# Kernel optimization log

Measured on AMD Instinct MI355X. Metric: run time of the kernel, lower is better.

Reference implementation:

```python
import jax, jax.numpy as jnp
import numpy as np

B, T, D_MODEL = 4, 8192, 1024
D_K, D_V = 128, 128
DILATIONS = [1, 2, 4, 8]
SEG = 128                      # segment_count for every head
NORM = 1.0 / np.sqrt(D_K)      # norm_fact = 1/sqrt(d_k)
H = len(DILATIONS)


def setup_inputs() -> dict:
    key = jax.random.key(0)
    ks = jax.random.split(key, 6)
    x = jax.random.normal(ks[0], (B, T, D_MODEL), dtype=jnp.float32)
    # head weights, init like torch: randn(k, m)/sqrt(k), stacked over heads
    Wk = jax.random.normal(ks[1], (H, D_K, D_MODEL), dtype=jnp.float32) / np.sqrt(D_K)
    Wq = jax.random.normal(ks[2], (H, D_K, D_MODEL), dtype=jnp.float32) / np.sqrt(D_K)
    Wv = jax.random.normal(ks[3], (H, D_V, D_MODEL), dtype=jnp.float32) / np.sqrt(D_V)
    # output projection (concat of H heads -> d_model), torch Linear layout (out, in)
    W_out = jax.random.normal(ks[4], (D_MODEL, H * D_V), dtype=jnp.float32) / np.sqrt(H * D_V)
    b_out = jnp.zeros((D_MODEL,), dtype=jnp.float32)
    return {"x": x, "Wk": Wk, "Wq": Wq, "Wv": Wv, "W_out": W_out, "b_out": b_out}


def _head(x, wk, wq, wv, dil):
    """SingleHeadDilatedSelfAttention with padding='same', is_causal=True."""
    Bb, Tt, E = x.shape
    nb = Tt // SEG                       # attention length before dilation
    # view(B, T//seg, seg, E).permute(0,2,3,1) -> (B, seg, E, nb); dilate last dim
    xv = x.reshape(Bb, nb, SEG, E).transpose(0, 2, 3, 1)[:, :, :, ::dil]  # (B, seg, E, L)
    Q = jnp.einsum('bsel,ke->bslk', xv, wq)   # (B, seg, L, d_k)
    K = jnp.einsum('bsel,ke->bslk', xv, wk)
    V = jnp.einsum('bsel,ve->bslv', xv, wv)   # (B, seg, L, d_v)
    # KQ[b,s,n,m]: n = key position, m = query position
    KQ = jnp.einsum('bsnd,bsmd->bsnm', K, Q)
    mask = jnp.tril(jnp.ones((nb, nb), dtype=bool))[::dil, ::dil]  # (L, L)
    KQ = jnp.where(mask, KQ, -jnp.inf)
    # original applies softmax along dim 3 (the query axis) of KQ * norm_fact
    smKQ = jax.nn.softmax(KQ * NORM, axis=3)
    att = jnp.einsum('bsnm,bsnv->bsmv', smKQ, V)   # (B, seg, L, d_v)
    L = att.shape[2]
    # 'same' padding: strided scatter back to full sequence length
    out = jnp.zeros((Bb, Tt, D_V), dtype=x.dtype)
    out = out.at[:, ::dil, :].set(att.reshape(Bb, SEG * L, D_V))
    return out


def reference(x, Wk, Wq, Wv, W_out, b_out):
    heads = [_head(x, Wk[h], Wq[h], Wv[h], DILATIONS[h]) for h in range(H)]
    cat = jnp.concatenate(heads, axis=-1)            # (B, T, H*d_v)
    return cat @ W_out.T + b_out                     # (B, T, d_model)
```

## Files before the change

### kernel.cpp

```cpp
#include <hip/hip_runtime.h>
#include <cstdint>
#include <cstddef>

typedef __attribute__((ext_vector_type(8))) short bf16x8;
typedef __attribute__((ext_vector_type(4))) float f32x4;

__device__ __forceinline__ unsigned short f2bf(float f) {
  union { float f; uint32_t u; } v; v.f = f;
  uint32_t r = v.u + 0x7fffu + ((v.u >> 16) & 1u);
  return (unsigned short)(r >> 16);
}
__device__ __forceinline__ float bf2f(unsigned short u) {
  union { uint32_t u; float f; } v; v.u = ((uint32_t)u) << 16;
  return v.f;
}

__device__ __forceinline__ void glds16(const void* g, void* l) {
  __builtin_amdgcn_global_load_lds(
      (const __attribute__((address_space(1))) unsigned int*)g,
      (__attribute__((address_space(3))) unsigned int*)l, 16, 0, 0);
}

__device__ __forceinline__ size_t head_off(int h) {
  return (size_t)65536 * ((h == 0) ? 0 : (h == 1) ? 64 : (h == 2) ? 96 : 112);
}

__global__ void k_cvt(const float* __restrict__ src, unsigned short* __restrict__ dst, int n4) {
  int i = blockIdx.x * 256 + threadIdx.x;
  if (i < n4) {
    float4 f = ((const float4*)src)[i];
    ushort4 u;
    u.x = f2bf(f.x); u.y = f2bf(f.y); u.z = f2bf(f.z); u.w = f2bf(f.w);
    ((ushort4*)dst)[i] = u;
  }
}

__global__ void k_cvt_w(const float* __restrict__ Wq, const float* __restrict__ Wk,
                        const float* __restrict__ Wv, unsigned short* __restrict__ dst) {
  int row = blockIdx.x;
  int h = row / 384, j = row % 384;
  const float* src = (j < 128) ? (Wq + (size_t)(h * 128 + j) * 1024)
                   : (j < 256) ? (Wk + (size_t)(h * 128 + j - 128) * 1024)
                               : (Wv + (size_t)(h * 128 + j - 256) * 1024);
  int e = threadIdx.x * 4;
  float4 f = *(const float4*)(src + e);
  ushort4 u;
  u.x = f2bf(f.x); u.y = f2bf(f.y); u.z = f2bf(f.z); u.w = f2bf(f.w);
  *(ushort4*)(dst + (size_t)row * 1024 + e) = u;
}

__global__ __launch_bounds__(256) void k_qkv(
    const unsigned short* __restrict__ xbf,
    const unsigned short* __restrict__ wbf,
    unsigned short* __restrict__ qws,
    unsigned short* __restrict__ kws,
    unsigned short* __restrict__ vws) {
  int i = blockIdx.x;
  int group = i / 24, jj = i - group * 24;
  int gy = jj >> 3, slot = jj & 7;
  int gx = group * 8 + slot;
  int h, base;
  if (gx < 256)      { h = 0; base = 0; }
  else if (gx < 384) { h = 1; base = 256; }
  else if (gx < 448) { h = 2; base = 384; }
  else               { h = 3; base = 448; }
  int L = 64 >> h, dil = 1 << h;
  int inner = gx - base;
  int b = inner >> (6 - h);
  int l = inner & (L - 1);
  const unsigned short* Abase = xbf + ((size_t)(b * 8192 + l * dil * 128)) * 1024;
  const unsigned short* Bbase = wbf + ((size_t)(h * 384 + gy * 128)) * 1024;

  __shared__ unsigned short As[128 * 64];
  __shared__ unsigned short Bs[128 * 64];

  int tid = threadIdx.x;
  int lane = tid & 63, wave = tid >> 6;
  int wm = wave >> 1, wn = wave & 1;
  int li = lane & 15, lk8 = (lane >> 4) << 3;

  int urow = tid >> 3;
  int uc8 = (tid & 7) << 3;

  f32x4 acc[4][4] = {};

  for (int kc = 0; kc < 1024; kc += 64) {
    __syncthreads();
#pragma unroll
    for (int it = 0; it < 4; ++it) {
      int row = it * 32 + urow;
      glds16(Abase + (size_t)row * 1024 + kc + uc8, &As[it * 2048 + wave * 512]);
      glds16(Bbase + (size_t)row * 1024 + kc + uc8, &Bs[it * 2048 + wave * 512]);
    }
    __syncthreads();
#pragma unroll
    for (int kk = 0; kk < 2; ++kk) {
      int k0 = kk * 32 + lk8;
      bf16x8 af[4], bfv[4];
#pragma unroll
      for (int mf = 0; mf < 4; ++mf)
        af[mf] = *(const bf16x8*)&As[(wm * 64 + mf * 16 + li) * 64 + k0];
#pragma unroll
      for (int nf = 0; nf < 4; ++nf)
        bfv[nf] = *(const bf16x8*)&Bs[(wn * 64 + nf * 16 + li) * 64 + k0];
#pragma unroll
      for (int mf = 0; mf < 4; ++mf)
#pragma unroll
        for (int nf = 0; nf < 4; ++nf)
          acc[mf][nf] = __builtin_amdgcn_mfma_f32_16x16x32_bf16(af[mf], bfv[nf], acc[mf][nf], 0, 0, 0);
    }
  }
  unsigned short* dst = ((gy == 0) ? qws : (gy == 1) ? kws : vws) + head_off(h);
  int ib = (lane >> 4) * 4;
#pragma unroll
  for (int mf = 0; mf < 4; ++mf) {
#pragma unroll
    for (int nf = 0; nf < 4; ++nf) {
#pragma unroll
      for (int rg = 0; rg < 4; ++rg) {
        int s = wm * 64 + mf * 16 + ib + rg;
        int j = wn * 64 + nf * 16 + li;
        dst[((size_t)((b * 128 + s) * L + l)) * 128 + j] = f2bf(acc[mf][nf][rg]);
      }
    }
  }
}

__global__ __launch_bounds__(256) void k_attn(
    const unsigned short* __restrict__ qws,
    const unsigned short* __restrict__ kws,
    const unsigned short* __restrict__ vws,
    unsigned short* __restrict__ att) {
  int bx = blockIdx.x;
  int h, inst;
  if (bx < 512)      { h = 0; inst = bx; }
  else if (bx < 768) { h = 1; inst = bx - 512; }
  else if (bx < 896) { h = 2; inst = bx - 768; }
  else               { h = 3; inst = bx - 896; }
  int lgL = 6 - h;
  int L = 64 >> h;
  int Lm1 = L - 1;
  int bpb = 128 >> h;
  int b = inst / bpb;
  int s0 = (inst % bpb) << h;
  size_t off0 = head_off(h) + ((size_t)(b * 128 + s0) * L) * 128;
  const unsigned short* Qg = qws + off0;
  const unsigned short* Kg = kws + off0;
  const unsigned short* Vg = vws + off0;
  unsigned short* Og = att + off0;

  __shared__ unsigned short PT[64][72];
  __shared__ unsigned short VtL[128][72];

  int tid = threadIdx.x;
  int lane = tid & 63, w = tid >> 6;
  int li = lane & 15, q = lane >> 4;
  int lk8 = q << 3;

#pragma unroll
  for (int c = 0; c < 4; ++c) {
    int u = tid + c * 256;
    int n = u & 63, vblk = u >> 6;
    bf16x8 ve = *(const bf16x8*)(Vg + n * 128 + vblk * 8);
#pragma unroll
    for (int j = 0; j < 8; ++j)
      VtL[vblk * 8 + j][n] = (unsigned short)ve[j];
  }

  f32x4 sacc[4] = {};
  int nrow = 16 * w + li;
  for (int kc = 0; kc < 4; ++kc) {
    int d0 = kc * 32 + lk8;
    bf16x8 af = *(const bf16x8*)(Kg + nrow * 128 + d0);
#pragma unroll
    for (int mt = 0; mt < 4; ++mt) {
      bf16x8 bfq = *(const bf16x8*)(Qg + (mt * 16 + li) * 128 + d0);
      sacc[mt] = __builtin_amdgcn_mfma_f32_16x16x32_bf16(af, bfq, sacc[mt], 0, 0, 0);
    }
  }

  float sv[4][4];
#pragma unroll
  for (int mt = 0; mt < 4; ++mt)
#pragma unroll
    for (int r = 0; r < 4; ++r) {
      int n = 16 * w + 4 * q + r;
      int m = mt * 16 + li;
      bool valid = ((m >> lgL) == (n >> lgL)) && ((m & Lm1) <= (n & Lm1));
      sv[mt][r] = valid ? sacc[mt][r] * 0.08838834764831845f : -1e30f;
    }
  float inv[4];
#pragma unroll
  for (int r = 0; r < 4; ++r) {
    float m0 = fmaxf(fmaxf(sv[0][r], sv[1][r]), fmaxf(sv[2][r], sv[3][r]));
#pragma unroll
    for (int d = 1; d < 16; d <<= 1)
      m0 = fmaxf(m0, __shfl_xor(m0, d, 64));
    float s0 = 0.f;
#pragma unroll
    for (int mt = 0; mt < 4; ++mt) {
      sv[mt][r] = __expf(sv[mt][r] - m0);
      s0 += sv[mt][r];
    }
#pragma unroll
    for (int d = 1; d < 16; d <<= 1)
      s0 += __shfl_xor(s0, d, 64);
    inv[r] = 1.f / s0;
  }

#pragma unroll
  for (int mt = 0; mt < 4; ++mt) {
    ushort4 pk;
    pk.x = f2bf(sv[mt][0] * inv[0]);
    pk.y = f2bf(sv[mt][1] * inv[1]);
    pk.z = f2bf(sv[mt][2] * inv[2]);
    pk.w = f2bf(sv[mt][3] * inv[3]);
    *(ushort4*)&PT[mt * 16 + li][16 * w + 4 * q] = pk;
  }
  __syncthreads();

  f32x4 oacc[8] = {};
#pragma unroll
  for (int ks = 0; ks < 2; ++ks) {
    int n0 = ks * 32 + lk8;
    bf16x8 af = *(const bf16x8*)&PT[16 * w + li][n0];
#pragma unroll
    for (int vt = 0; vt < 8; ++vt) {
      bf16x8 bfv = *(const bf16x8*)&VtL[vt * 16 + li][n0];
      oacc[vt] = __builtin_amdgcn_mfma_f32_16x16x32_bf16(af, bfv, oacc[vt], 0, 0, 0);
    }
  }
#pragma unroll
  for (int vt = 0; vt < 8; ++vt) {
#pragma unroll
    for (int r = 0; r < 4; ++r) {
      int m = 16 * w + 4 * q + r;
      int v = vt * 16 + li;
      Og[m * 128 + v] = f2bf(oacc[vt][r]);
    }
  }
}

__global__ __launch_bounds__(256) void k_out(
    const unsigned short* __restrict__ att,
    const unsigned short* __restrict__ wout,
    const float* __restrict__ bout,
    float* __restrict__ out) {
  int mt = blockIdx.x, nt = blockIdx.y;
  int row0 = mt * 128;

  __shared__ unsigned short As[128 * 64];
  __shared__ unsigned short Bs[128 * 64];

  int tid = threadIdx.x;
  int lane = tid & 63, wave = tid >> 6;
  int wm = wave >> 1, wn = wave & 1;
  int li = lane & 15, lk8 = (lane >> 4) << 3;

  int urow = tid >> 3;
  int uc8 = (tid & 7) << 3;
  const bf16x8 ZV = {0, 0, 0, 0, 0, 0, 0, 0};

  f32x4 acc[4][4] = {};

  for (int kc = 0; kc < 512; kc += 64) {
    int hd = kc >> 7;
    int dil = 1 << hd, Lh = 64 >> hd, v0 = kc & 127;
    __syncthreads();
#pragma unroll
    for (int it = 0; it < 4; ++it) {
      int row = it * 32 + urow;
      glds16(wout + (size_t)(nt * 128 + row) * 512 + kc + uc8, &Bs[it * 2048 + wave * 512]);
    }
#pragma unroll
    for (int it = 0; it < 4; ++it) {
      int row = it * 32 + urow;
      int rg = row0 + row;
      int b = rg >> 13, t = rg & 8191;
      if ((t & (dil - 1)) == 0) {
        int j2 = t >> hd;
        int s = j2 >> (6 - hd), l2 = j2 & (Lh - 1);
        glds16(att + head_off(hd) + ((size_t)((b * 128 + s) * Lh + l2)) * 128 + v0 + uc8,
               &As[it * 2048 + wave * 512]);
      } else {
        *(bf16x8*)&As[it * 2048 + wave * 512 + lane * 8] = ZV;
      }
    }
    __syncthreads();
#pragma unroll
    for (int kk = 0; kk < 2; ++kk) {
      int k0 = kk * 32 + lk8;
      bf16x8 af[4], bfv[4];
#pragma unroll
      for (int mf = 0; mf < 4; ++mf)
        af[mf] = *(const bf16x8*)&As[(wm * 64 + mf * 16 + li) * 64 + k0];
#pragma unroll
      for (int nf = 0; nf < 4; ++nf)
        bfv[nf] = *(const bf16x8*)&Bs[(wn * 64 + nf * 16 + li) * 64 + k0];
#pragma unroll
      for (int mf = 0; mf < 4; ++mf)
#pragma unroll
        for (int nf = 0; nf < 4; ++nf)
          acc[mf][nf] = __builtin_amdgcn_mfma_f32_16x16x32_bf16(af[mf], bfv[nf], acc[mf][nf], 0, 0, 0);
    }
  }
  int ib = (lane >> 4) * 4;
#pragma unroll
  for (int mf = 0; mf < 4; ++mf) {
#pragma unroll
    for (int nf = 0; nf < 4; ++nf) {
      int col = nt * 128 + wn * 64 + nf * 16 + li;
      float bo = bout[col];
#pragma unroll
      for (int rg = 0; rg < 4; ++rg) {
        int r = row0 + wm * 64 + mf * 16 + ib + rg;
        out[(size_t)r * 1024 + col] = acc[mf][nf][rg] + bo;
      }
    }
  }
}

extern "C" void kernel_launch(void* const* d_in, const int* in_sizes, int n_in,
                              void* d_out, int out_size, void* d_ws, size_t ws_size,
                              hipStream_t stream) {
  const float* x  = (const float*)d_in[0];
  const float* Wk = (const float*)d_in[1];
  const float* Wq = (const float*)d_in[2];
  const float* Wv = (const float*)d_in[3];
  const float* Wo = (const float*)d_in[4];
  const float* bo = (const float*)d_in[5];
  float* out = (float*)d_out;
  char* ws = (char*)d_ws;
  unsigned short* xbf  = (unsigned short*)(ws);
  unsigned short* wbf  = (unsigned short*)(ws + 67108864);
  unsigned short* wobf = (unsigned short*)(ws + 70254592);
  unsigned short* qws  = (unsigned short*)(ws + 71303168);
  unsigned short* kws  = (unsigned short*)(ws + 87031808);
  unsigned short* vws  = (unsigned short*)(ws + 102760448);
  unsigned short* attw = (unsigned short*)(ws + 118489088);

  k_cvt<<<dim3(32768), dim3(256), 0, stream>>>(x, xbf, 8388608);
  k_cvt_w<<<dim3(1536), dim3(256), 0, stream>>>(Wq, Wk, Wv, wbf);
  k_cvt<<<dim3(512), dim3(256), 0, stream>>>(Wo, wobf, 131072);
  k_qkv<<<dim3(1440), dim3(256), 0, stream>>>(xbf, wbf, qws, kws, vws);
  k_attn<<<dim3(960), dim3(256), 0, stream>>>(qws, kws, vws, attw);
  k_out<<<dim3(256, 8), dim3(256), 0, stream>>>(attw, wobf, bo, out);
}
```

Baseline: 375.3 us.

## Double-buffer LDS in QKV and output GEMMs and remap QKV blocks for x reuse

```diff
diff --git a/kernel.cpp b/kernel.cpp
--- a/kernel.cpp
+++ b/kernel.cpp
@@ -56,23 +56,21 @@
     unsigned short* __restrict__ kws,
     unsigned short* __restrict__ vws) {
   int i = blockIdx.x;
-  int group = i / 24, jj = i - group * 24;
-  int gy = jj >> 3, slot = jj & 7;
-  int gx = group * 8 + slot;
-  int h, base;
-  if (gx < 256)      { h = 0; base = 0; }
-  else if (gx < 384) { h = 1; base = 256; }
-  else if (gx < 448) { h = 2; base = 384; }
-  else               { h = 3; base = 448; }
-  int L = 64 >> h, dil = 1 << h;
-  int inner = gx - base;
-  int b = inner >> (6 - h);
-  int l = inner & (L - 1);
-  const unsigned short* Abase = xbf + ((size_t)(b * 8192 + l * dil * 128)) * 1024;
-  const unsigned short* Bbase = wbf + ((size_t)(h * 384 + gy * 128)) * 1024;
-
-  __shared__ unsigned short As[128 * 64];
-  __shared__ unsigned short Bs[128 * 64];
+  int bid = (i & 7) * 180 + (i >> 3);
+  int b = bid / 360, r = bid - b * 360;
+  int g, v;
+  if (r < 96)        { int q = r / 3;              g = 2 * q + 1; v = r - q * 3; }
+  else if (r < 192)  { int rr = r - 96;  int q = rr / 6;  g = 4 * q + 2; v = rr - q * 6; }
+  else if (r < 264)  { int rr = r - 192; int q = rr / 9;  g = 8 * q + 4; v = rr - q * 9; }
+  else               { int rr = r - 264; int q = rr / 12; g = 8 * q;     v = rr - q * 12; }
+  int h = v / 3, mat = v - (v / 3) * 3;
+  int l = g >> h;
+  int L = 64 >> h;
+  const unsigned short* Abase = xbf + ((size_t)(b * 8192 + g * 128)) * 1024;
+  const unsigned short* Bbase = wbf + ((size_t)(h * 384 + mat * 128)) * 1024;
+
+  __shared__ unsigned short As[2][128 * 64];
+  __shared__ unsigned short Bs[2][128 * 64];
 
   int tid = threadIdx.x;
   int lane = tid & 63, wave = tid >> 6;
@@ -82,35 +80,43 @@
   int urow = tid >> 3;
   int uc8 = (tid & 7) << 3;
 
+#define QKV_STAGE(BUF, KCOL)                                                         \
+  _Pragma("unroll")                                                                  \
+  for (int it = 0; it < 4; ++it) {                                                   \
+    int row = it * 32 + urow;                                                        \
+    glds16(Abase + (size_t)row * 1024 + (KCOL) + uc8, &As[BUF][it * 2048 + wave * 512]); \
+    glds16(Bbase + (size_t)row * 1024 + (KCOL) + uc8, &Bs[BUF][it * 2048 + wave * 512]); \
+  }
+
   f32x4 acc[4][4] = {};
 
-  for (int kc = 0; kc < 1024; kc += 64) {
-    __syncthreads();
-#pragma unroll
-    for (int it = 0; it < 4; ++it) {
-      int row = it * 32 + urow;
-      glds16(Abase + (size_t)row * 1024 + kc + uc8, &As[it * 2048 + wave * 512]);
-      glds16(Bbase + (size_t)row * 1024 + kc + uc8, &Bs[it * 2048 + wave * 512]);
-    }
-    __syncthreads();
+  QKV_STAGE(0, 0)
+  __syncthreads();
+
+  for (int t = 0; t < 16; ++t) {
+    int cur = t & 1;
+    if (t < 15) { QKV_STAGE(cur ^ 1, (t + 1) * 64) }
 #pragma unroll
     for (int kk = 0; kk < 2; ++kk) {
       int k0 = kk * 32 + lk8;
       bf16x8 af[4], bfv[4];
 #pragma unroll
       for (int mf = 0; mf < 4; ++mf)
-        af[mf] = *(const bf16x8*)&As[(wm * 64 + mf * 16 + li) * 64 + k0];
+        af[mf] = *(const bf16x8*)&As[cur][(wm * 64 + mf * 16 + li) * 64 + k0];
 #pragma unroll
       for (int nf = 0; nf < 4; ++nf)
-        bfv[nf] = *(const bf16x8*)&Bs[(wn * 64 + nf * 16 + li) * 64 + k0];
+        bfv[nf] = *(const bf16x8*)&Bs[cur][(wn * 64 + nf * 16 + li) * 64 + k0];
 #pragma unroll
       for (int mf = 0; mf < 4; ++mf)
 #pragma unroll
         for (int nf = 0; nf < 4; ++nf)
           acc[mf][nf] = __builtin_amdgcn_mfma_f32_16x16x32_bf16(af[mf], bfv[nf], acc[mf][nf], 0, 0, 0);
     }
-  }
-  unsigned short* dst = ((gy == 0) ? qws : (gy == 1) ? kws : vws) + head_off(h);
+    __syncthreads();
+  }
+#undef QKV_STAGE
+
+  unsigned short* dst = ((mat == 0) ? qws : (mat == 1) ? kws : vws) + head_off(h);
   int ib = (lane >> 4) * 4;
 #pragma unroll
   for (int mf = 0; mf < 4; ++mf) {
@@ -249,8 +255,8 @@
   int mt = blockIdx.x, nt = blockIdx.y;
   int row0 = mt * 128;
 
-  __shared__ unsigned short As[128 * 64];
-  __shared__ unsigned short Bs[128 * 64];
+  __shared__ unsigned short As[2][128 * 64];
+  __shared__ unsigned short Bs[2][128 * 64];
 
   int tid = threadIdx.x;
   int lane = tid & 63, wave = tid >> 6;
@@ -261,49 +267,60 @@
   int uc8 = (tid & 7) << 3;
   const bf16x8 ZV = {0, 0, 0, 0, 0, 0, 0, 0};
 
+#define OUT_STAGE(BUF, KCOL)                                                          \
+  {                                                                                   \
+    int hd = (KCOL) >> 7;                                                             \
+    int dil = 1 << hd, Lh = 64 >> hd, v0 = (KCOL) & 127;                              \
+    _Pragma("unroll")                                                                 \
+    for (int it = 0; it < 4; ++it) {                                                  \
+      int row = it * 32 + urow;                                                       \
+      glds16(wout + (size_t)(nt * 128 + row) * 512 + (KCOL) + uc8,                    \
+             &Bs[BUF][it * 2048 + wave * 512]);                                       \
+    }                                                                                 \
+    _Pragma("unroll")                                                                 \
+    for (int it = 0; it < 4; ++it) {                                                  \
+      int row = it * 32 + urow;                                                       \
+      int rg = row0 + row;                                                            \
+      int b2 = rg >> 13, tt = rg & 8191;                                              \
+      if ((tt & (dil - 1)) == 0) {                                                    \
+        int j2 = tt >> hd;                                                            \
+        int s = j2 >> (6 - hd), l2 = j2 & (Lh - 1);                                   \
+        glds16(att + head_off(hd) + ((size_t)((b2 * 128 + s) * Lh + l2)) * 128 + v0 + uc8, \
+               &As[BUF][it * 2048 + wave * 512]);                                     \
+      } else {                                                                        \
+        *(bf16x8*)&As[BUF][it * 2048 + wave * 512 + lane * 8] = ZV;                   \
+      }                                                                               \
+    }                                                                                 \
+  }
+
   f32x4 acc[4][4] = {};
 
-  for (int kc = 0; kc < 512; kc += 64) {
-    int hd = kc >> 7;
-    int dil = 1 << hd, Lh = 64 >> hd, v0 = kc & 127;
-    __syncthreads();
-#pragma unroll
-    for (int it = 0; it < 4; ++it) {
-      int row = it * 32 + urow;
-      glds16(wout + (size_t)(nt * 128 + row) * 512 + kc + uc8, &Bs[it * 2048 + wave * 512]);
-    }
-#pragma unroll
-    for (int it = 0; it < 4; ++it) {
-      int row = it * 32 + urow;
-      int rg = row0 + row;
-      int b = rg >> 13, t = rg & 8191;
-      if ((t & (dil - 1)) == 0) {
-        int j2 = t >> hd;
-        int s = j2 >> (6 - hd), l2 = j2 & (Lh - 1);
-        glds16(att + head_off(hd) + ((size_t)((b * 128 + s) * Lh + l2)) * 128 + v0 + uc8,
-               &As[it * 2048 + wave * 512]);
-      } else {
-        *(bf16x8*)&As[it * 2048 + wave * 512 + lane * 8] = ZV;
-      }
-    }
-    __syncthreads();
+  OUT_STAGE(0, 0)
+  __syncthreads();
+
+  for (int t = 0; t < 8; ++t) {
+    int cur = t & 1;
+    if (t < 7) { OUT_STAGE(cur ^ 1, (t + 1) * 64) }
 #pragma unroll
     for (int kk = 0; kk < 2; ++kk) {
       int k0 = kk * 32 + lk8;
       bf16x8 af[4], bfv[4];
 #pragma unroll
       for (int mf = 0; mf < 4; ++mf)
-        af[mf] = *(const bf16x8*)&As[(wm * 64 + mf * 16 + li) * 64 + k0];
+        af[mf] = *(const bf16x8*)&As[cur][(wm * 64 + mf * 16 + li) * 64 + k0];
 #pragma unroll
       for (int nf = 0; nf < 4; ++nf)
-        bfv[nf] = *(const bf16x8*)&Bs[(wn * 64 + nf * 16 + li) * 64 + k0];
+        bfv[nf] = *(const bf16x8*)&Bs[cur][(wn * 64 + nf * 16 + li) * 64 + k0];
 #pragma unroll
       for (int mf = 0; mf < 4; ++mf)
 #pragma unroll
         for (int nf = 0; nf < 4; ++nf)
           acc[mf][nf] = __builtin_amdgcn_mfma_f32_16x16x32_bf16(af[mf], bfv[nf], acc[mf][nf], 0, 0, 0);
     }
-  }
+    __syncthreads();
+  }
+#undef OUT_STAGE
+
   int ib = (lane >> 4) * 4;
 #pragma unroll
   for (int mf = 0; mf < 4; ++mf) {
```

After: 394.6 us. 5.1% more time.
